# Optimization experiments

Hardware: AMD Instinct MI355X
Metric: run time of the kernel (lower is better)

Reference implementation:

```python
import jax, jax.numpy as jnp
import numpy as np

D_MODEL = 1024
N_LAYERS = 4
D_INNER = 2 * D_MODEL          # expand=2
D_STATE = 16
D_CONV = 4
DT_RANK = D_MODEL // 16        # ceil(1024/16)=64
B, T = 2, 1024


def setup_inputs() -> dict:
    key = jax.random.key(0)
    ks = jax.random.split(key, 8)
    s = 0.02
    return {
        "x": jax.random.normal(ks[0], (B, T, D_MODEL), jnp.float32),
        "in_proj_w": jax.random.normal(ks[1], (N_LAYERS, 2 * D_INNER, D_MODEL), jnp.float32) * s,
        "conv_w": jax.random.normal(ks[2], (N_LAYERS, D_INNER, D_CONV), jnp.float32) * s,
        "conv_b": jnp.zeros((N_LAYERS, D_INNER), jnp.float32),
        "x_proj_w": jax.random.normal(ks[3], (N_LAYERS, DT_RANK + 2 * D_STATE, D_INNER), jnp.float32) * s,
        "dt_proj_w": jax.random.normal(ks[4], (N_LAYERS, D_INNER, DT_RANK), jnp.float32) * s,
        "dt_proj_b": jax.random.normal(ks[5], (N_LAYERS, D_INNER), jnp.float32) * 0.1,
        "A_log": jnp.tile(jnp.log(jnp.arange(1.0, D_STATE + 1.0, dtype=jnp.float32)), (N_LAYERS, D_INNER, 1)),
        "Dd": jnp.ones((N_LAYERS, D_INNER), jnp.float32),
        "out_proj_w": jax.random.normal(ks[6], (N_LAYERS, D_MODEL, D_INNER), jnp.float32) * s,
        "norm_w": jnp.ones((D_MODEL,), jnp.float32),
        "norm_b": jnp.zeros((D_MODEL,), jnp.float32),
    }


def _silu(v):
    return v * jax.nn.sigmoid(v)


def _mamba_block(x, in_w, cw, cb, xp_w, dtp_w, dtp_b, A_log, Dv, out_w):
    # x: [B,T,d_model]
    xz = jnp.einsum('btd,ed->bte', x, in_w)            # [B,T,2*d_inner]
    u, z = jnp.split(xz, 2, axis=-1)                   # each [B,T,d_inner]
    # causal depthwise conv over time
    uc = jax.lax.conv_general_dilated(
        u.transpose(0, 2, 1),                          # [B,d_inner,T]
        cw[:, None, :],                                # [d_inner,1,K]
        window_strides=(1,), padding=[(D_CONV - 1, 0)],
        feature_group_count=D_INNER,
        dimension_numbers=('NCH', 'OIH', 'NCH'))
    uc = _silu(uc.transpose(0, 2, 1) + cb)             # [B,T,d_inner]
    x_dbl = jnp.einsum('btd,ed->bte', uc, xp_w)        # [B,T,dt_rank+2*d_state]
    dt_r = x_dbl[..., :DT_RANK]
    Bm = x_dbl[..., DT_RANK:DT_RANK + D_STATE]         # [B,T,d_state]
    Cm = x_dbl[..., DT_RANK + D_STATE:]                # [B,T,d_state]
    dt = jax.nn.softplus(jnp.einsum('btr,dr->btd', dt_r, dtp_w) + dtp_b)  # [B,T,d_inner]
    A = -jnp.exp(A_log)                                # [d_inner,d_state]

    def step(h, inp):
        u_t, dt_t, B_t, C_t = inp                      # [B,dI],[B,dI],[B,dS],[B,dS]
        h = jnp.exp(dt_t[..., None] * A) * h + (dt_t * u_t)[..., None] * B_t[:, None, :]
        return h, jnp.einsum('bds,bs->bd', h, C_t)

    h0 = jnp.zeros((x.shape[0], D_INNER, D_STATE), x.dtype)
    xs = (uc.transpose(1, 0, 2), dt.transpose(1, 0, 2), Bm.transpose(1, 0, 2), Cm.transpose(1, 0, 2))
    _, ys = jax.lax.scan(step, h0, xs)                 # ys: [T,B,d_inner]
    y = ys.transpose(1, 0, 2) + uc * Dv                # skip term D*u
    y = y * _silu(z)                                   # gated
    return jnp.einsum('btd,ed->bte', y, out_w)         # [B,T,d_model]


def reference(x, in_proj_w, conv_w, conv_b, x_proj_w, dt_proj_w, dt_proj_b, A_log, Dd, out_proj_w, norm_w, norm_b):
    for i in range(in_proj_w.shape[0]):
        residual = x
        x = _mamba_block(x, in_proj_w[i], conv_w[i], conv_b[i], x_proj_w[i],
                         dt_proj_w[i], dt_proj_b[i], A_log[i], Dd[i], out_proj_w[i])
        x = x + residual
    mu = jnp.mean(x, -1, keepdims=True)
    var = jnp.var(x, -1, keepdims=True)
    return (x - mu) / jnp.sqrt(var + 1e-5) * norm_w + norm_b
```

## Files before the change

### kernel.cpp

```cpp
#include <hip/hip_runtime.h>
#include <hip/hip_bf16.h>

#define N_LAYERS 4
#define D_MODEL  1024
#define D_INNER  2048
#define D_STATE  16
#define D_CONV   4
#define DT_RANK  64
#define BB       2
#define TT       1024
#define BT       (BB*TT)

#define NCHUNK 32
#define SCTC   (TT/NCHUNK)
#define TB     8

#define XP_KS  8

typedef unsigned short ushort_t;
typedef __attribute__((ext_vector_type(8))) short short8;
typedef __attribute__((ext_vector_type(4))) float f32x4;

__device__ __forceinline__ float sigmoidf_(float x){ return 1.f/(1.f+__expf(-x)); }
__device__ __forceinline__ float siluf_(float x){ return x*sigmoidf_(x); }
__device__ __forceinline__ float softplusf_(float x){ return fmaxf(x,0.f) + log1pf(__expf(-fabsf(x))); }
__device__ __forceinline__ ushort_t f2b(float f){
    unsigned int x = __builtin_bit_cast(unsigned int, f);
    unsigned int r = (x + 0x7fffu + ((x>>16)&1u)) >> 16;
    return (ushort_t)r;
}
__device__ __forceinline__ float b2f(ushort_t u){
    unsigned int x = ((unsigned int)u) << 16;
    return __builtin_bit_cast(float, x);
}

#define GLOAD(g, l) __builtin_amdgcn_global_load_lds( \
    (const __attribute__((address_space(1))) void*)(g), \
    (__attribute__((address_space(3))) void*)(l), 16, 0, 0)

__global__ __launch_bounds__(256) void f2ball_k(
    const float* __restrict__ x, const float* __restrict__ in_w,
    const float* __restrict__ out_w, const float* __restrict__ dtp_w,
    ushort_t* __restrict__ xinb, ushort_t* __restrict__ winb,
    ushort_t* __restrict__ woutb, ushort_t* __restrict__ dtpb)
{
    const int n0 = (BT*1024)/4;
    const int n1 = (N_LAYERS*4096*1024)/4;
    const int n2 = (N_LAYERS*1024*2048)/4;
    int i = blockIdx.x*256 + threadIdx.x;
    const float4* src; ushort4* dst; int j;
    if (i < n0){ src=(const float4*)x; dst=(ushort4*)xinb; j=i; }
    else if (i < n0+n1){ src=(const float4*)in_w; dst=(ushort4*)winb; j=i-n0; }
    else if (i < n0+n1+n2){ src=(const float4*)out_w; dst=(ushort4*)woutb; j=i-n0-n1; }
    else { src=(const float4*)dtp_w; dst=(ushort4*)dtpb; j=i-n0-n1-n2; }
    float4 v = src[j];
    ushort4 o;
    o.x = f2b(v.x); o.y = f2b(v.y); o.z = f2b(v.z); o.w = f2b(v.w);
    dst[j] = o;
}

__global__ __launch_bounds__(512) void gemm_ip(
    const ushort_t* __restrict__ A, const ushort_t* __restrict__ W,
    int M, int N, int K, ushort_t* __restrict__ outb,
    int RM, int RN, int XN)
{
    __shared__ ushort_t As[4][128*32];
    __shared__ ushort_t Ws[4][128*32];
    const int tid  = threadIdx.x;
    const int lane = tid & 63;
    const int wv   = tid >> 6;
    const int wm0  = (wv>>2)*64, wn0 = (wv&3)*32;

    const int bid = blockIdx.x;
    const int xcd = bid & 7, bi = bid >> 3;
    const int xm = xcd / XN, xn = xcd - xm*XN;
    const int m0 = (xm*RM + bi/RN)*128;
    const int n0 = (xn*RN + bi - (bi/RN)*RN)*128;

    const int r0 = tid>>2, ch = tid&3;

    f32x4 acc[4][2];
    #pragma unroll
    for (int i=0;i<4;++i)
        #pragma unroll
        for (int j=0;j<2;++j) acc[i][j] = (f32x4){0.f,0.f,0.f,0.f};

    const int row_a = lane & 15, kc = (lane>>4)*8;
    const ushort_t* gA = A + (size_t)(m0+r0)*K + ch*8;
    const ushort_t* gW = W + (size_t)(n0+r0)*K + ch*8;

#define STAGE(KT, BUF) { \
    GLOAD(gA + (KT)*32, (char*)&As[BUF][0] + tid*16); \
    GLOAD(gW + (KT)*32, (char*)&Ws[BUF][0] + tid*16); }

#define COMPUTE(BUF) { \
    short8 af[4], bf[2]; \
    _Pragma("unroll") \
    for (int i=0;i<4;++i) af[i] = *(const short8*)&As[BUF][(wm0 + i*16 + row_a)*32 + kc]; \
    _Pragma("unroll") \
    for (int j=0;j<2;++j) bf[j] = *(const short8*)&Ws[BUF][(wn0 + j*16 + row_a)*32 + kc]; \
    __builtin_amdgcn_s_setprio(1); \
    _Pragma("unroll") \
    for (int i=0;i<4;++i) \
        _Pragma("unroll") \
        for (int j=0;j<2;++j) \
            acc[i][j] = __builtin_amdgcn_mfma_f32_16x16x32_bf16(af[i], bf[j], acc[i][j], 0,0,0); \
    __builtin_amdgcn_s_setprio(0); }

    const int nt = K >> 5;
    STAGE(0, 0); STAGE(1, 1); STAGE(2, 2);
    for (int t = 0; t < nt-3; ++t){
        asm volatile("s_waitcnt vmcnt(4)" ::: "memory");
        asm volatile("s_barrier" ::: "memory");
        STAGE(t+3, (t+3)&3);
        COMPUTE(t&3);
    }
    asm volatile("s_waitcnt vmcnt(4)" ::: "memory");
    asm volatile("s_barrier" ::: "memory");
    COMPUTE((nt-3)&3);
    asm volatile("s_waitcnt vmcnt(2)" ::: "memory");
    asm volatile("s_barrier" ::: "memory");
    COMPUTE((nt-2)&3);
    asm volatile("s_waitcnt vmcnt(0)" ::: "memory");
    asm volatile("s_barrier" ::: "memory");
    COMPUTE((nt-1)&3);
#undef STAGE
#undef COMPUTE

    const int crow = (lane>>4)*4, ccol = lane & 15;
    #pragma unroll
    for (int i=0;i<4;++i){
        #pragma unroll
        for (int j=0;j<2;++j){
            #pragma unroll
            for (int r=0;r<4;++r){
                int m = m0 + wm0 + i*16 + crow + r;
                int n = n0 + wn0 + j*16 + ccol;
                outb[(size_t)m*N + n] = f2b(acc[i][j][r]);
            }
        }
    }
}

__global__ __launch_bounds__(256) void gemm_op(
    const ushort_t* __restrict__ A, const ushort_t* __restrict__ W,
    float* __restrict__ C, int M, int N, int K,
    const float* __restrict__ res, ushort_t* __restrict__ outb,
    int RM, int RN, int XN)
{
    __shared__ ushort_t As[6][64*32];
    __shared__ ushort_t Ws[6][64*32];
    const int tid  = threadIdx.x;
    const int lane = tid & 63;
    const int wv   = tid >> 6;
    const int wm0  = (wv>>1)*32, wn0 = (wv&1)*32;

    const int bid = blockIdx.x;
    const int xcd = bid & 7, bi = bid >> 3;
    const int xm = xcd / XN, xn = xcd - xm*XN;
    const int m0 = (xm*RM + bi/RN)*64;
    const int n0 = (xn*RN + bi - (bi/RN)*RN)*64;

    const int r0 = tid>>2, ch = tid&3;

    f32x4 acc[2][2];
    #pragma unroll
    for (int i=0;i<2;++i)
        #pragma unroll
        for (int j=0;j<2;++j) acc[i][j] = (f32x4){0.f,0.f,0.f,0.f};

    const int row_a = lane & 15, kc = (lane>>4)*8;
    const ushort_t* gA = A + (size_t)(m0+r0)*K + ch*8;
    const ushort_t* gW = W + (size_t)(n0+r0)*K + ch*8;

#define STAGE(KT, BUF) { \
    GLOAD(gA + (KT)*32, (char*)&As[BUF][0] + tid*16); \
    GLOAD(gW + (KT)*32, (char*)&Ws[BUF][0] + tid*16); }

#define COMPUTE(BUF) { \
    short8 af[2], bf[2]; \
    _Pragma("unroll") \
    for (int i=0;i<2;++i) af[i] = *(const short8*)&As[BUF][(wm0 + i*16 + row_a)*32 + kc]; \
    _Pragma("unroll") \
    for (int j=0;j<2;++j) bf[j] = *(const short8*)&Ws[BUF][(wn0 + j*16 + row_a)*32 + kc]; \
    _Pragma("unroll") \
    for (int i=0;i<2;++i) \
        _Pragma("unroll") \
        for (int j=0;j<2;++j) \
            acc[i][j] = __builtin_amdgcn_mfma_f32_16x16x32_bf16(af[i], bf[j], acc[i][j], 0,0,0); }

    const int np = K >> 6;
    STAGE(0, 0); STAGE(1, 1);
    STAGE(2, 2); STAGE(3, 3);
    for (int p = 0; p < np-2; ++p){
        const int bA = (p%3)*2, bS = ((p+2)%3)*2;
        asm volatile("s_waitcnt vmcnt(4)" ::: "memory");
        asm volatile("s_barrier" ::: "memory");
        STAGE(2*p+4, bS); STAGE(2*p+5, bS+1);
        __builtin_amdgcn_s_setprio(1);
        COMPUTE(bA); COMPUTE(bA+1);
        __builtin_amdgcn_s_setprio(0);
    }
    {
        const int bA = ((np-2)%3)*2;
        asm volatile("s_waitcnt vmcnt(4)" ::: "memory");
        asm volatile("s_barrier" ::: "memory");
        COMPUTE(bA); COMPUTE(bA+1);
    }
    {
        const int bA = ((np-1)%3)*2;
        asm volatile("s_waitcnt vmcnt(0)" ::: "memory");
        asm volatile("s_barrier" ::: "memory");
        COMPUTE(bA); COMPUTE(bA+1);
    }
#undef STAGE
#undef COMPUTE

    const int crow = (lane>>4)*4, ccol = lane & 15;
    #pragma unroll
    for (int i=0;i<2;++i){
        #pragma unroll
        for (int j=0;j<2;++j){
            #pragma unroll
            for (int r=0;r<4;++r){
                int m = m0 + wm0 + i*16 + crow + r;
                int n = n0 + wn0 + j*16 + ccol;
                float v = acc[i][j][r] + res[(size_t)m*N + n];
                C[(size_t)m*N + n] = v;
                outb[(size_t)m*N + n] = f2b(v);
            }
        }
    }
}

__global__ __launch_bounds__(256) void dt_mfma(
    const ushort_t* __restrict__ A, const ushort_t* __restrict__ W,
    const float* __restrict__ bias, ushort_t* __restrict__ dtb, int N)
{
    __shared__ ushort_t As[2][64*32];
    __shared__ ushort_t Ws[2][64*32];
    const int tid = threadIdx.x, lane = tid&63, wv = tid>>6;
    const int wm0 = (wv>>1)*32, wn0 = (wv&1)*32;
    const int m0 = blockIdx.y*64, n0 = blockIdx.x*64;
    const int r0 = tid>>2, ch = tid&3;
    const ushort_t* gA = A + (size_t)(m0+r0)*64 + ch*8;
    const ushort_t* gW = W + (size_t)(n0+r0)*64 + ch*8;
    GLOAD(gA,      (char*)&As[0][0] + tid*16);
    GLOAD(gW,      (char*)&Ws[0][0] + tid*16);
    GLOAD(gA + 32, (char*)&As[1][0] + tid*16);
    GLOAD(gW + 32, (char*)&Ws[1][0] + tid*16);

    f32x4 acc[2][2];
    #pragma unroll
    for (int i=0;i<2;++i)
        #pragma unroll
        for (int j=0;j<2;++j) acc[i][j] = (f32x4){0.f,0.f,0.f,0.f};

    asm volatile("s_waitcnt vmcnt(0)" ::: "memory");
    asm volatile("s_barrier" ::: "memory");
    const int row_a = lane&15, kc = (lane>>4)*8;
    #pragma unroll
    for (int buf=0; buf<2; ++buf){
        short8 af[2], bf[2];
        #pragma unroll
        for (int i=0;i<2;++i) af[i] = *(const short8*)&As[buf][(wm0 + i*16 + row_a)*32 + kc];
        #pragma unroll
        for (int j=0;j<2;++j) bf[j] = *(const short8*)&Ws[buf][(wn0 + j*16 + row_a)*32 + kc];
        #pragma unroll
        for (int i=0;i<2;++i)
            #pragma unroll
            for (int j=0;j<2;++j)
                acc[i][j] = __builtin_amdgcn_mfma_f32_16x16x32_bf16(af[i], bf[j], acc[i][j], 0,0,0);
    }

    const int crow = (lane>>4)*4, ccol = lane & 15;
    #pragma unroll
    for (int i=0;i<2;++i){
        #pragma unroll
        for (int j=0;j<2;++j){
            #pragma unroll
            for (int r=0;r<4;++r){
                int m = m0 + wm0 + i*16 + crow + r;
                int n = n0 + wn0 + j*16 + ccol;
                float v = softplusf_(acc[i][j][r] + bias[n]);
                dtb[(size_t)m*N + n] = f2b(v);
            }
        }
    }
}

__global__ __launch_bounds__(256) void gemm_tn_sk(
    const ushort_t* __restrict__ xzb, const float* __restrict__ cw,
    const float* __restrict__ cb,
    const float* __restrict__ W, int ldw,
    float* __restrict__ P, int M, int N, int K)
{
    __shared__ float As[16][68];
    __shared__ float Ws[16][68];
    const int tid = threadIdx.x;
    const int tx = tid & 15, ty = tid >> 4;
    const int m0 = blockIdx.y * 64, n0 = blockIdx.x * 64;
    const int kbase = blockIdx.z * (K/XP_KS);
    const int lr = tid >> 2;
    const int lk = (tid & 3) << 2;
    float acc[4][4] = {{0.f}};
    const int m = m0 + lr;
    const int t = m & (TT-1);

    for (int kk = 0; kk < K/XP_KS; kk += 16) {
        const int k0 = kbase + kk;
        const int colb = k0 + lk;
        ushort4 z4; z4.x=0; z4.y=0; z4.z=0; z4.w=0;
        ushort4 xr0 = (t >= 3) ? *(const ushort4*)(xzb + (size_t)(m-3)*4096 + colb) : z4;
        ushort4 xr1 = (t >= 2) ? *(const ushort4*)(xzb + (size_t)(m-2)*4096 + colb) : z4;
        ushort4 xr2 = (t >= 1) ? *(const ushort4*)(xzb + (size_t)(m-1)*4096 + colb) : z4;
        ushort4 xr3 = *(const ushort4*)(xzb + (size_t)m*4096 + colb);
        const ushort_t* q0 = (const ushort_t*)&xr0;
        const ushort_t* q1 = (const ushort_t*)&xr1;
        const ushort_t* q2 = (const ushort_t*)&xr2;
        const ushort_t* q3 = (const ushort_t*)&xr3;
        float av[4];
        #pragma unroll
        for (int jj=0;jj<4;++jj){
            float4 w4 = *(const float4*)(cw + (size_t)(colb+jj)*4);
            float a = cb[colb+jj];
            a = fmaf(b2f(q0[jj]), w4.x, a);
            a = fmaf(b2f(q1[jj]), w4.y, a);
            a = fmaf(b2f(q2[jj]), w4.z, a);
            a = fmaf(b2f(q3[jj]), w4.w, a);
            av[jj] = siluf_(a);
        }
        float4 wvv = make_float4(0.f,0.f,0.f,0.f);
        if (n0 + lr < N) wvv = *(const float4*)(W + (size_t)(n0+lr)*ldw + k0 + lk);
        __syncthreads();
        As[lk+0][lr]=av[0]; As[lk+1][lr]=av[1]; As[lk+2][lr]=av[2]; As[lk+3][lr]=av[3];
        Ws[lk+0][lr]=wvv.x; Ws[lk+1][lr]=wvv.y; Ws[lk+2][lr]=wvv.z; Ws[lk+3][lr]=wvv.w;
        __syncthreads();
        #pragma unroll
        for (int k = 0; k < 16; ++k) {
            float4 a = *(const float4*)&As[k][ty<<2];
            float4 b = *(const float4*)&Ws[k][tx<<2];
            float a4[4] = {a.x,a.y,a.z,a.w};
            float b4[4] = {b.x,b.y,b.z,b.w};
            #pragma unroll
            for (int i=0;i<4;++i)
                #pragma unroll
                for (int j=0;j<4;++j)
                    acc[i][j] = fmaf(a4[i], b4[j], acc[i][j]);
        }
    }

    float* Pz = P + (size_t)blockIdx.z * M * 96;
    #pragma unroll
    for (int i=0;i<4;++i){
        int mm = m0 + (ty<<2) + i;
        #pragma unroll
        for (int j=0;j<4;++j){
            int n = n0 + (tx<<2) + j;
            if (n < N) Pz[(size_t)mm*96 + n] = acc[i][j];
        }
    }
}

__global__ __launch_bounds__(256) void sk_reduce(
    const float* __restrict__ P, float* __restrict__ outp,
    ushort_t* __restrict__ dtrb, int MN)
{
    int g = blockIdx.x*256 + threadIdx.x;
    float s = 0.f;
    #pragma unroll
    for (int ks=0; ks<XP_KS; ++ks) s += P[(size_t)ks*MN + g];
    outp[g] = s;
    int m = g / 96, c = g - m*96;
    if (c < 64) dtrb[(size_t)m*64 + c] = f2b(s);
}


__global__ __launch_bounds__(256) void scan_p1(
    const ushort_t* __restrict__ dt, const ushort_t* __restrict__ xzb,
    const float* __restrict__ cw, const float* __restrict__ cb,
    const float* __restrict__ xdbl, const float* __restrict__ A_log,
    float* __restrict__ hpart, float* __restrict__ hdecay)
{
    const int tid = threadIdx.x;
    const int d = blockIdx.x*256 + tid;
    const int b = blockIdx.y;
    const int k = blockIdx.z;
    const int t0 = k*SCTC;
    float A[16];
    #pragma unroll
    for (int q=0;q<4;++q){
        float4 v = *(const float4*)(A_log + (size_t)d*16 + q*4);
        A[q*4+0]=-__expf(v.x); A[q*4+1]=-__expf(v.y);
        A[q*4+2]=-__expf(v.z); A[q*4+3]=-__expf(v.w);
    }
    float h[16];
    #pragma unroll
    for (int s=0;s<16;++s) h[s]=0.f;
    float sumdt = 0.f;
    const ushort_t* dtp = dt + ((size_t)b*TT + t0)*D_INNER + d;
    const ushort_t* up  = xzb + ((size_t)b*TT + t0)*4096 + d;
    const float* bcp = xdbl + ((size_t)b*TT + t0)*96 + 64;
    float4 w4 = *(const float4*)(cw + (size_t)d*4);
    const float cbd = cb[d];
    float u3=0.f, u2=0.f, u1=0.f;
    if (t0 > 0){
        u3 = b2f(*(up - 3*4096));
        u2 = b2f(*(up - 2*4096));
        u1 = b2f(*(up - 4096));
    }
    #pragma unroll
    for (int tb=0; tb<SCTC; tb+=TB){
        float dtv[TB], ur[TB];
        #pragma unroll
        for (int j=0;j<TB;++j){
            dtv[j] = b2f(dtp[(size_t)(tb+j)*D_INNER]);
            ur[j]  = b2f(up [(size_t)(tb+j)*4096]);
        }
        #pragma unroll
        for (int j=0;j<TB;++j){
            float uv = siluf_(fmaf(ur[j],w4.w, fmaf(u1,w4.z, fmaf(u2,w4.y, fmaf(u3,w4.x, cbd)))));
            u3=u2; u2=u1; u1=ur[j];
            const float* bc = bcp + (size_t)(tb+j)*96;
            float du = dtv[j]*uv;
            sumdt += dtv[j];
            #pragma unroll
            for (int s=0;s<16;++s)
                h[s] = fmaf(__expf(dtv[j]*A[s]), h[s], du*bc[s]);
        }
    }
    size_t base = ((size_t)(k*BB+b)*D_INNER + d)*16;
    float4* hp = (float4*)(hpart + base);
    float4* hd = (float4*)(hdecay + base);
    #pragma unroll
    for (int q=0;q<4;++q){
        hp[q] = make_float4(h[q*4],h[q*4+1],h[q*4+2],h[q*4+3]);
        hd[q] = make_float4(__expf(sumdt*A[q*4+0]),__expf(sumdt*A[q*4+1]),
                            __expf(sumdt*A[q*4+2]),__expf(sumdt*A[q*4+3]));
    }
}

__global__ __launch_bounds__(256) void scan_fix(
    const float* __restrict__ hpart, const float* __restrict__ hdecay,
    float* __restrict__ hstart)
{
    int g = blockIdx.x*256 + threadIdx.x;
    float h = 0.f;
    #pragma unroll
    for (int k=0;k<NCHUNK;++k){
        size_t idx = (size_t)k*(BB*D_INNER*16) + g;
        hstart[idx] = h;
        h = fmaf(hdecay[idx], h, hpart[idx]);
    }
}

__global__ __launch_bounds__(256) void scan_p3(
    const ushort_t* __restrict__ dt, const ushort_t* __restrict__ xzb,
    const float* __restrict__ cw, const float* __restrict__ cb,
    const float* __restrict__ xdbl, const float* __restrict__ A_log,
    const float* __restrict__ Dd, const float* __restrict__ hstart,
    ushort_t* __restrict__ ysb)
{
    const int tid = threadIdx.x;
    const int d = blockIdx.x*256 + tid;
    const int b = blockIdx.y;
    const int k = blockIdx.z;
    const int t0 = k*SCTC;
    float A[16];
    #pragma unroll
    for (int q=0;q<4;++q){
        float4 v = *(const float4*)(A_log + (size_t)d*16 + q*4);
        A[q*4+0]=-__expf(v.x); A[q*4+1]=-__expf(v.y);
        A[q*4+2]=-__expf(v.z); A[q*4+3]=-__expf(v.w);
    }
    float h[16];
    {
        const float4* hs = (const float4*)(hstart + ((size_t)(k*BB+b)*D_INNER + d)*16);
        #pragma unroll
        for (int q=0;q<4;++q){
            float4 v = hs[q];
            h[q*4+0]=v.x; h[q*4+1]=v.y; h[q*4+2]=v.z; h[q*4+3]=v.w;
        }
    }
    const float Ddc = Dd[d];
    const ushort_t* dtp = dt + ((size_t)b*TT + t0)*D_INNER + d;
    const ushort_t* up  = xzb + ((size_t)b*TT + t0)*4096 + d;
    const ushort_t* zp  = xzb + ((size_t)b*TT + t0)*4096 + 2048 + d;
    const float* bcp = xdbl + ((size_t)b*TT + t0)*96 + 64;
    ushort_t* yp = ysb + ((size_t)b*TT + t0)*D_INNER + d;
    float4 w4 = *(const float4*)(cw + (size_t)d*4);
    const float cbd = cb[d];
    float u3=0.f, u2=0.f, u1=0.f;
    if (t0 > 0){
        u3 = b2f(*(up - 3*4096));
        u2 = b2f(*(up - 2*4096));
        u1 = b2f(*(up - 4096));
    }
    #pragma unroll
    for (int tb=0; tb<SCTC; tb+=TB){
        float dtv[TB], ur[TB], zr[TB];
        #pragma unroll
        for (int j=0;j<TB;++j){
            dtv[j] = b2f(dtp[(size_t)(tb+j)*D_INNER]);
            ur[j]  = b2f(up [(size_t)(tb+j)*4096]);
            zr[j]  = b2f(zp [(size_t)(tb+j)*4096]);
        }
        #pragma unroll
        for (int j=0;j<TB;++j){
            float uv = siluf_(fmaf(ur[j],w4.w, fmaf(u1,w4.z, fmaf(u2,w4.y, fmaf(u3,w4.x, cbd)))));
            u3=u2; u2=u1; u1=ur[j];
            const float* bc = bcp + (size_t)(tb+j)*96;
            float du = dtv[j]*uv;
            float y0=0.f,y1=0.f,y2=0.f,y3=0.f;
            #pragma unroll
            for (int q=0;q<4;++q){
                h[q*4+0] = fmaf(__expf(dtv[j]*A[q*4+0]), h[q*4+0], du*bc[q*4+0]);
                h[q*4+1] = fmaf(__expf(dtv[j]*A[q*4+1]), h[q*4+1], du*bc[q*4+1]);
                h[q*4+2] = fmaf(__expf(dtv[j]*A[q*4+2]), h[q*4+2], du*bc[q*4+2]);
                h[q*4+3] = fmaf(__expf(dtv[j]*A[q*4+3]), h[q*4+3], du*bc[q*4+3]);
            }
            #pragma unroll
            for (int q=0;q<4;++q){
                y0 = fmaf(h[q*4+0], bc[16+q*4+0], y0);
                y1 = fmaf(h[q*4+1], bc[16+q*4+1], y1);
                y2 = fmaf(h[q*4+2], bc[16+q*4+2], y2);
                y3 = fmaf(h[q*4+3], bc[16+q*4+3], y3);
            }
            float y = (y0+y1)+(y2+y3);
            float yv = (y + uv*Ddc) * siluf_(zr[j]);
            yp[(size_t)(tb+j)*D_INNER] = f2b(yv);
        }
    }
}

__global__ __launch_bounds__(256) void layernorm_k(
    const float* __restrict__ X, const float* __restrict__ w,
    const float* __restrict__ b, float* __restrict__ out)
{
    int row = blockIdx.x;
    int tid = threadIdx.x;
    const float* xr = X + (size_t)row*D_MODEL;
    float4 v = *(const float4*)(xr + tid*4);
    float s  = v.x+v.y+v.z+v.w;
    float ss = fmaf(v.x,v.x, fmaf(v.y,v.y, fmaf(v.z,v.z, v.w*v.w)));
    #pragma unroll
    for (int off=32; off>0; off>>=1){
        s  += __shfl_down(s, off, 64);
        ss += __shfl_down(ss, off, 64);
    }
    __shared__ float red[8];
    int wid = tid>>6, lane = tid&63;
    if (lane==0){ red[wid]=s; red[4+wid]=ss; }
    __syncthreads();
    if (tid==0){
        float S  = red[0]+red[1]+red[2]+red[3];
        float SS = red[4]+red[5]+red[6]+red[7];
        float mu = S*(1.f/D_MODEL);
        float var = SS*(1.f/D_MODEL) - mu*mu;
        red[0]=mu; red[1]=rsqrtf(var + 1e-5f);
    }
    __syncthreads();
    float mu=red[0], rs=red[1];
    float4 wv = *(const float4*)(w + tid*4);
    float4 bv = *(const float4*)(b + tid*4);
    float4 o;
    o.x = fmaf((v.x-mu)*rs, wv.x, bv.x);
    o.y = fmaf((v.y-mu)*rs, wv.y, bv.y);
    o.z = fmaf((v.z-mu)*rs, wv.z, bv.z);
    o.w = fmaf((v.w-mu)*rs, wv.w, bv.w);
    *(float4*)(out + (size_t)row*D_MODEL + tid*4) = o;
}

extern "C" void kernel_launch(void* const* d_in, const int* in_sizes, int n_in,
                              void* d_out, int out_size, void* d_ws, size_t ws_size,
                              hipStream_t stream) {
    (void)in_sizes; (void)n_in; (void)out_size; (void)ws_size;
    const float* x      = (const float*)d_in[0];
    const float* in_w   = (const float*)d_in[1];
    const float* conv_w = (const float*)d_in[2];
    const float* conv_b = (const float*)d_in[3];
    const float* xp_w   = (const float*)d_in[4];
    const float* dtp_w  = (const float*)d_in[5];
    const float* dtp_b  = (const float*)d_in[6];
    const float* A_log  = (const float*)d_in[7];
    const float* Dd     = (const float*)d_in[8];
    const float* out_w  = (const float*)d_in[9];
    const float* nw     = (const float*)d_in[10];
    const float* nb     = (const float*)d_in[11];
    float* out = (float*)d_out;

    char* p = (char*)d_ws;
    ushort_t* xzb  = (ushort_t*)p; p += (size_t)BT*4096*2;
    float* xdbl    = (float*)p;  p += (size_t)BT*96*4;
    ushort_t* dtrb = (ushort_t*)p; p += (size_t)BT*64*2;
    ushort_t* dtbb = (ushort_t*)p; p += (size_t)BT*2048*2;
    float* xcur    = (float*)p;  p += (size_t)BT*1024*4;
    ushort_t* xinb = (ushort_t*)p; p += (size_t)BT*1024*2;
    ushort_t* ysb  = (ushort_t*)p; p += (size_t)BT*2048*2;
    ushort_t* winb = (ushort_t*)p; p += (size_t)N_LAYERS*4096*1024*2;
    ushort_t* woutb= (ushort_t*)p; p += (size_t)N_LAYERS*1024*2048*2;
    ushort_t* dtpb = (ushort_t*)p; p += (size_t)N_LAYERS*2048*64*2;
    float* hpart   = (float*)p;  p += (size_t)NCHUNK*BB*D_INNER*16*4;
    float* hdecay  = (float*)p;  p += (size_t)NCHUNK*BB*D_INNER*16*4;
    float* hstart  = (float*)p;  p += (size_t)NCHUNK*BB*D_INNER*16*4;
    float* pbuf    = hpart;

    f2ball_k<<<(BT*1024 + N_LAYERS*(4096*1024 + 1024*2048 + 2048*64))/1024,
               256,0,stream>>>(x, in_w, out_w, dtp_w, xinb, winb, woutb, dtpb);

    for (int i = 0; i < N_LAYERS; ++i){
        const float* xin = (i==0) ? x : xcur;
        const float* cw = conv_w + (size_t)i*D_INNER*D_CONV;
        const float* cb = conv_b + (size_t)i*D_INNER;
        gemm_ip<<<512,512,0,stream>>>(
            xinb, winb + (size_t)i*4096*1024, BT, 4096, D_MODEL, xzb, 8, 8, 4);
        gemm_tn_sk<<<dim3(2,32,XP_KS),256,0,stream>>>(
            xzb, cw, cb, xp_w + (size_t)i*96*D_INNER, D_INNER,
            pbuf, BT, 96, D_INNER);
        sk_reduce<<<(BT*96)/256,256,0,stream>>>(pbuf, xdbl, dtrb, BT*96);
        dt_mfma<<<dim3(D_INNER/64, BT/64),256,0,stream>>>(
            dtrb, dtpb + (size_t)i*2048*64, dtp_b + (size_t)i*D_INNER, dtbb, D_INNER);
        scan_p1<<<dim3(D_INNER/256, BB, NCHUNK),256,0,stream>>>(
            dtbb, xzb, cw, cb, xdbl, A_log + (size_t)i*D_INNER*D_STATE,
            hpart, hdecay);
        scan_fix<<<(BB*D_INNER*16)/256,256,0,stream>>>(hpart, hdecay, hstart);
        scan_p3<<<dim3(D_INNER/256, BB, NCHUNK),256,0,stream>>>(
            dtbb, xzb, cw, cb, xdbl, A_log + (size_t)i*D_INNER*D_STATE,
            Dd + (size_t)i*D_INNER, hstart, ysb);
        gemm_op<<<512,256,0,stream>>>(
            ysb, woutb + (size_t)i*1024*2048, xcur, BT, 1024, D_INNER,
            xin, xinb, 8, 8, 2);
    }
    layernorm_k<<<BT,256,0,stream>>>(xcur, nw, nb, out);
}
```

Baseline: 727.4 us.

## Materialize conv+SiLU output once instead of recomputing in three kernels

Adds a dedicated conv_silu kernel that computes the causal depthwise conv plus SiLU once per layer and writes a bf16 buffer. The x_proj GEMM and both scan passes now read this buffer instead of each recomputing the conv from xz. The goal is to remove the redundant conv work, the extra strided loads of the previous three timesteps, and the sigmoid in the scan and GEMM inner loops. In exchange it adds a kernel launch plus an 8 MB write and reread per layer, and rounds the conv output to bf16, which slightly changes numerics. The fp32-to-bf16 cast kernel is also widened to process 8 elements per thread.

Result: faster. 681.8 us (median of 2 runs) (-6.3%).

```diff
diff --git a/kernel.cpp b/kernel.cpp
--- a/kernel.cpp
+++ b/kernel.cpp
@@ -19,6 +19,7 @@
 
 typedef unsigned short ushort_t;
 typedef __attribute__((ext_vector_type(8))) short short8;
+typedef __attribute__((ext_vector_type(8))) unsigned short ushort8_t;
 typedef __attribute__((ext_vector_type(4))) float f32x4;
 
 __device__ __forceinline__ float sigmoidf_(float x){ return 1.f/(1.f+__expf(-x)); }
@@ -44,18 +45,19 @@
     ushort_t* __restrict__ xinb, ushort_t* __restrict__ winb,
     ushort_t* __restrict__ woutb, ushort_t* __restrict__ dtpb)
 {
-    const int n0 = (BT*1024)/4;
-    const int n1 = (N_LAYERS*4096*1024)/4;
-    const int n2 = (N_LAYERS*1024*2048)/4;
+    const int n0 = (BT*1024)/8;
+    const int n1 = (N_LAYERS*4096*1024)/8;
+    const int n2 = (N_LAYERS*1024*2048)/8;
     int i = blockIdx.x*256 + threadIdx.x;
-    const float4* src; ushort4* dst; int j;
-    if (i < n0){ src=(const float4*)x; dst=(ushort4*)xinb; j=i; }
-    else if (i < n0+n1){ src=(const float4*)in_w; dst=(ushort4*)winb; j=i-n0; }
-    else if (i < n0+n1+n2){ src=(const float4*)out_w; dst=(ushort4*)woutb; j=i-n0-n1; }
-    else { src=(const float4*)dtp_w; dst=(ushort4*)dtpb; j=i-n0-n1-n2; }
-    float4 v = src[j];
-    ushort4 o;
-    o.x = f2b(v.x); o.y = f2b(v.y); o.z = f2b(v.z); o.w = f2b(v.w);
+    const float4* src; ushort8_t* dst; int j;
+    if (i < n0){ src=(const float4*)x; dst=(ushort8_t*)xinb; j=i; }
+    else if (i < n0+n1){ src=(const float4*)in_w; dst=(ushort8_t*)winb; j=i-n0; }
+    else if (i < n0+n1+n2){ src=(const float4*)out_w; dst=(ushort8_t*)woutb; j=i-n0-n1; }
+    else { src=(const float4*)dtp_w; dst=(ushort8_t*)dtpb; j=i-n0-n1-n2; }
+    float4 v0 = src[2*j], v1 = src[2*j+1];
+    ushort8_t o;
+    o[0]=f2b(v0.x); o[1]=f2b(v0.y); o[2]=f2b(v0.z); o[3]=f2b(v0.w);
+    o[4]=f2b(v1.x); o[5]=f2b(v1.y); o[6]=f2b(v1.z); o[7]=f2b(v1.w);
     dst[j] = o;
 }
 
@@ -289,9 +291,35 @@
     }
 }
 
+__global__ __launch_bounds__(256) void conv_silu_k(
+    const ushort_t* __restrict__ xzb, const float* __restrict__ cw,
+    const float* __restrict__ cb, ushort_t* __restrict__ ucb)
+{
+    int idx = blockIdx.x*256 + threadIdx.x;
+    int d8 = (idx & 255) << 3;
+    int bt = idx >> 8;
+    int t  = bt & (TT-1);
+    ushort8_t z8 = (ushort8_t)0;
+    ushort8_t r0 = (t>=3) ? *(const ushort8_t*)(xzb + (size_t)(bt-3)*4096 + d8) : z8;
+    ushort8_t r1 = (t>=2) ? *(const ushort8_t*)(xzb + (size_t)(bt-2)*4096 + d8) : z8;
+    ushort8_t r2 = (t>=1) ? *(const ushort8_t*)(xzb + (size_t)(bt-1)*4096 + d8) : z8;
+    ushort8_t r3 = *(const ushort8_t*)(xzb + (size_t)bt*4096 + d8);
+    ushort8_t o;
+    #pragma unroll
+    for (int j=0;j<8;++j){
+        float4 w4 = *(const float4*)(cw + (size_t)(d8+j)*4);
+        float a = cb[d8+j];
+        a = fmaf(b2f(r0[j]), w4.x, a);
+        a = fmaf(b2f(r1[j]), w4.y, a);
+        a = fmaf(b2f(r2[j]), w4.z, a);
+        a = fmaf(b2f(r3[j]), w4.w, a);
+        o[j] = f2b(siluf_(a));
+    }
+    *(ushort8_t*)(ucb + (size_t)bt*D_INNER + d8) = o;
+}
+
 __global__ __launch_bounds__(256) void gemm_tn_sk(
-    const ushort_t* __restrict__ xzb, const float* __restrict__ cw,
-    const float* __restrict__ cb,
+    const ushort_t* __restrict__ A, int lda,
     const float* __restrict__ W, int ldw,
     float* __restrict__ P, int M, int N, int K)
 {
@@ -304,37 +332,16 @@
     const int lr = tid >> 2;
     const int lk = (tid & 3) << 2;
     float acc[4][4] = {{0.f}};
-    const int m = m0 + lr;
-    const int t = m & (TT-1);
 
     for (int kk = 0; kk < K/XP_KS; kk += 16) {
-        const int k0 = kbase + kk;
-        const int colb = k0 + lk;
-        ushort4 z4; z4.x=0; z4.y=0; z4.z=0; z4.w=0;
-        ushort4 xr0 = (t >= 3) ? *(const ushort4*)(xzb + (size_t)(m-3)*4096 + colb) : z4;
-        ushort4 xr1 = (t >= 2) ? *(const ushort4*)(xzb + (size_t)(m-2)*4096 + colb) : z4;
-        ushort4 xr2 = (t >= 1) ? *(const ushort4*)(xzb + (size_t)(m-1)*4096 + colb) : z4;
-        ushort4 xr3 = *(const ushort4*)(xzb + (size_t)m*4096 + colb);
-        const ushort_t* q0 = (const ushort_t*)&xr0;
-        const ushort_t* q1 = (const ushort_t*)&xr1;
-        const ushort_t* q2 = (const ushort_t*)&xr2;
-        const ushort_t* q3 = (const ushort_t*)&xr3;
-        float av[4];
-        #pragma unroll
-        for (int jj=0;jj<4;++jj){
-            float4 w4 = *(const float4*)(cw + (size_t)(colb+jj)*4);
-            float a = cb[colb+jj];
-            a = fmaf(b2f(q0[jj]), w4.x, a);
-            a = fmaf(b2f(q1[jj]), w4.y, a);
-            a = fmaf(b2f(q2[jj]), w4.z, a);
-            a = fmaf(b2f(q3[jj]), w4.w, a);
-            av[jj] = siluf_(a);
-        }
-        float4 wvv = make_float4(0.f,0.f,0.f,0.f);
-        if (n0 + lr < N) wvv = *(const float4*)(W + (size_t)(n0+lr)*ldw + k0 + lk);
+        int k0 = kbase + kk;
+        ushort4 av4 = *(const ushort4*)(A + (size_t)(m0+lr)*lda + k0 + lk);
+        float4 wv = make_float4(0.f,0.f,0.f,0.f);
+        if (n0 + lr < N) wv = *(const float4*)(W + (size_t)(n0+lr)*ldw + k0 + lk);
         __syncthreads();
-        As[lk+0][lr]=av[0]; As[lk+1][lr]=av[1]; As[lk+2][lr]=av[2]; As[lk+3][lr]=av[3];
-        Ws[lk+0][lr]=wvv.x; Ws[lk+1][lr]=wvv.y; Ws[lk+2][lr]=wvv.z; Ws[lk+3][lr]=wvv.w;
+        As[lk+0][lr]=b2f(av4.x); As[lk+1][lr]=b2f(av4.y);
+        As[lk+2][lr]=b2f(av4.z); As[lk+3][lr]=b2f(av4.w);
+        Ws[lk+0][lr]=wv.x; Ws[lk+1][lr]=wv.y; Ws[lk+2][lr]=wv.z; Ws[lk+3][lr]=wv.w;
         __syncthreads();
         #pragma unroll
         for (int k = 0; k < 16; ++k) {
@@ -353,11 +360,11 @@
     float* Pz = P + (size_t)blockIdx.z * M * 96;
     #pragma unroll
     for (int i=0;i<4;++i){
-        int mm = m0 + (ty<<2) + i;
+        int m = m0 + (ty<<2) + i;
         #pragma unroll
         for (int j=0;j<4;++j){
             int n = n0 + (tx<<2) + j;
-            if (n < N) Pz[(size_t)mm*96 + n] = acc[i][j];
+            if (n < N) Pz[(size_t)m*96 + n] = acc[i][j];
         }
     }
 }
@@ -377,8 +384,7 @@
 
 
 __global__ __launch_bounds__(256) void scan_p1(
-    const ushort_t* __restrict__ dt, const ushort_t* __restrict__ xzb,
-    const float* __restrict__ cw, const float* __restrict__ cb,
+    const ushort_t* __restrict__ dt, const ushort_t* __restrict__ uc,
     const float* __restrict__ xdbl, const float* __restrict__ A_log,
     float* __restrict__ hpart, float* __restrict__ hdecay)
 {
@@ -399,30 +405,20 @@
     for (int s=0;s<16;++s) h[s]=0.f;
     float sumdt = 0.f;
     const ushort_t* dtp = dt + ((size_t)b*TT + t0)*D_INNER + d;
-    const ushort_t* up  = xzb + ((size_t)b*TT + t0)*4096 + d;
+    const ushort_t* ucp = uc + ((size_t)b*TT + t0)*D_INNER + d;
     const float* bcp = xdbl + ((size_t)b*TT + t0)*96 + 64;
-    float4 w4 = *(const float4*)(cw + (size_t)d*4);
-    const float cbd = cb[d];
-    float u3=0.f, u2=0.f, u1=0.f;
-    if (t0 > 0){
-        u3 = b2f(*(up - 3*4096));
-        u2 = b2f(*(up - 2*4096));
-        u1 = b2f(*(up - 4096));
-    }
     #pragma unroll
     for (int tb=0; tb<SCTC; tb+=TB){
         float dtv[TB], ur[TB];
         #pragma unroll
         for (int j=0;j<TB;++j){
             dtv[j] = b2f(dtp[(size_t)(tb+j)*D_INNER]);
-            ur[j]  = b2f(up [(size_t)(tb+j)*4096]);
+            ur[j]  = b2f(ucp[(size_t)(tb+j)*D_INNER]);
         }
         #pragma unroll
         for (int j=0;j<TB;++j){
-            float uv = siluf_(fmaf(ur[j],w4.w, fmaf(u1,w4.z, fmaf(u2,w4.y, fmaf(u3,w4.x, cbd)))));
-            u3=u2; u2=u1; u1=ur[j];
             const float* bc = bcp + (size_t)(tb+j)*96;
-            float du = dtv[j]*uv;
+            float du = dtv[j]*ur[j];
             sumdt += dtv[j];
             #pragma unroll
             for (int s=0;s<16;++s)
@@ -455,11 +451,10 @@
 }
 
 __global__ __launch_bounds__(256) void scan_p3(
-    const ushort_t* __restrict__ dt, const ushort_t* __restrict__ xzb,
-    const float* __restrict__ cw, const float* __restrict__ cb,
+    const ushort_t* __restrict__ dt, const ushort_t* __restrict__ uc,
     const float* __restrict__ xdbl, const float* __restrict__ A_log,
-    const float* __restrict__ Dd, const float* __restrict__ hstart,
-    ushort_t* __restrict__ ysb)
+    const ushort_t* __restrict__ xzb, const float* __restrict__ Dd,
+    const float* __restrict__ hstart, ushort_t* __restrict__ ysb)
 {
     const int tid = threadIdx.x;
     const int d = blockIdx.x*256 + tid;
@@ -484,33 +479,23 @@
     }
     const float Ddc = Dd[d];
     const ushort_t* dtp = dt + ((size_t)b*TT + t0)*D_INNER + d;
-    const ushort_t* up  = xzb + ((size_t)b*TT + t0)*4096 + d;
+    const ushort_t* ucp = uc + ((size_t)b*TT + t0)*D_INNER + d;
     const ushort_t* zp  = xzb + ((size_t)b*TT + t0)*4096 + 2048 + d;
     const float* bcp = xdbl + ((size_t)b*TT + t0)*96 + 64;
     ushort_t* yp = ysb + ((size_t)b*TT + t0)*D_INNER + d;
-    float4 w4 = *(const float4*)(cw + (size_t)d*4);
-    const float cbd = cb[d];
-    float u3=0.f, u2=0.f, u1=0.f;
-    if (t0 > 0){
-        u3 = b2f(*(up - 3*4096));
-        u2 = b2f(*(up - 2*4096));
-        u1 = b2f(*(up - 4096));
-    }
     #pragma unroll
     for (int tb=0; tb<SCTC; tb+=TB){
         float dtv[TB], ur[TB], zr[TB];
         #pragma unroll
         for (int j=0;j<TB;++j){
             dtv[j] = b2f(dtp[(size_t)(tb+j)*D_INNER]);
-            ur[j]  = b2f(up [(size_t)(tb+j)*4096]);
+            ur[j]  = b2f(ucp[(size_t)(tb+j)*D_INNER]);
             zr[j]  = b2f(zp [(size_t)(tb+j)*4096]);
         }
         #pragma unroll
         for (int j=0;j<TB;++j){
-            float uv = siluf_(fmaf(ur[j],w4.w, fmaf(u1,w4.z, fmaf(u2,w4.y, fmaf(u3,w4.x, cbd)))));
-            u3=u2; u2=u1; u1=ur[j];
             const float* bc = bcp + (size_t)(tb+j)*96;
-            float du = dtv[j]*uv;
+            float du = dtv[j]*ur[j];
             float y0=0.f,y1=0.f,y2=0.f,y3=0.f;
             #pragma unroll
             for (int q=0;q<4;++q){
@@ -527,7 +512,7 @@
                 y3 = fmaf(h[q*4+3], bc[16+q*4+3], y3);
             }
             float y = (y0+y1)+(y2+y3);
-            float yv = (y + uv*Ddc) * siluf_(zr[j]);
+            float yv = (y + ur[j]*Ddc) * siluf_(zr[j]);
             yp[(size_t)(tb+j)*D_INNER] = f2b(yv);
         }
     }
@@ -591,6 +576,7 @@
 
     char* p = (char*)d_ws;
     ushort_t* xzb  = (ushort_t*)p; p += (size_t)BT*4096*2;
+    ushort_t* ucb  = (ushort_t*)p; p += (size_t)BT*2048*2;
     float* xdbl    = (float*)p;  p += (size_t)BT*96*4;
     ushort_t* dtrb = (ushort_t*)p; p += (size_t)BT*64*2;
     ushort_t* dtbb = (ushort_t*)p; p += (size_t)BT*2048*2;
@@ -605,7 +591,7 @@
     float* hstart  = (float*)p;  p += (size_t)NCHUNK*BB*D_INNER*16*4;
     float* pbuf    = hpart;
 
-    f2ball_k<<<(BT*1024 + N_LAYERS*(4096*1024 + 1024*2048 + 2048*64))/1024,
+    f2ball_k<<<(BT*1024 + N_LAYERS*(4096*1024 + 1024*2048 + 2048*64))/2048,
                256,0,stream>>>(x, in_w, out_w, dtp_w, xinb, winb, woutb, dtpb);
 
     for (int i = 0; i < N_LAYERS; ++i){
@@ -614,18 +600,18 @@
         const float* cb = conv_b + (size_t)i*D_INNER;
         gemm_ip<<<512,512,0,stream>>>(
             xinb, winb + (size_t)i*4096*1024, BT, 4096, D_MODEL, xzb, 8, 8, 4);
+        conv_silu_k<<<BT,256,0,stream>>>(xzb, cw, cb, ucb);
         gemm_tn_sk<<<dim3(2,32,XP_KS),256,0,stream>>>(
-            xzb, cw, cb, xp_w + (size_t)i*96*D_INNER, D_INNER,
+            ucb, D_INNER, xp_w + (size_t)i*96*D_INNER, D_INNER,
             pbuf, BT, 96, D_INNER);
         sk_reduce<<<(BT*96)/256,256,0,stream>>>(pbuf, xdbl, dtrb, BT*96);
         dt_mfma<<<dim3(D_INNER/64, BT/64),256,0,stream>>>(
             dtrb, dtpb + (size_t)i*2048*64, dtp_b + (size_t)i*D_INNER, dtbb, D_INNER);
         scan_p1<<<dim3(D_INNER/256, BB, NCHUNK),256,0,stream>>>(
-            dtbb, xzb, cw, cb, xdbl, A_log + (size_t)i*D_INNER*D_STATE,
-            hpart, hdecay);
+            dtbb, ucb, xdbl, A_log + (size_t)i*D_INNER*D_STATE, hpart, hdecay);
         scan_fix<<<(BB*D_INNER*16)/256,256,0,stream>>>(hpart, hdecay, hstart);
         scan_p3<<<dim3(D_INNER/256, BB, NCHUNK),256,0,stream>>>(
-            dtbb, xzb, cw, cb, xdbl, A_log + (size_t)i*D_INNER*D_STATE,
+            dtbb, ucb, xdbl, A_log + (size_t)i*D_INNER*D_STATE, xzb,
             Dd + (size_t)i*D_INNER, hstart, ysb);
         gemm_op<<<512,256,0,stream>>>(
             ysb, woutb + (size_t)i*1024*2048, xcur, BT, 1024, D_INNER,
```
